# Kernel optimization log

Measured on AMD Instinct MI355X. Metric: run time of the kernel, lower is better.

The kernel has to match this reference:

```python
import jax, jax.numpy as jnp
import numpy as np

NUM_HEADS = 16


def setup_inputs() -> dict:
    key = jax.random.key(0)
    ks = jax.random.split(key, 6)
    B, N, M, C = 2, 2048, 2048, 1024
    return {
        "reference_data": jax.random.normal(ks[0], (B, N, C), dtype=jnp.float32),
        "target_data": jax.random.normal(ks[1], (B, M, C), dtype=jnp.float32),
        "Wq": jax.random.normal(ks[2], (C, C), dtype=jnp.float32) * (C ** -0.5),
        "Wkv": jax.random.normal(ks[3], (C, 2 * C), dtype=jnp.float32) * (C ** -0.5),
        "Wproj": jax.random.normal(ks[4], (C, C), dtype=jnp.float32) * (C ** -0.5),
        "bproj": jnp.zeros((C,), dtype=jnp.float32),
    }


def reference(reference_data, target_data, Wq, Wkv, Wproj, bproj):
    B, N, C = reference_data.shape
    M = target_data.shape[1]
    H = NUM_HEADS
    hd = C // H
    scale = hd ** -0.5
    # k, v from reference: [B, N, 2, H, hd] -> two [B, H, N, hd]
    kv = (reference_data @ Wkv).reshape(B, N, 2, H, hd)
    k = jnp.transpose(kv[:, :, 0], (0, 2, 1, 3))  # [B,H,N,hd]
    v = jnp.transpose(kv[:, :, 1], (0, 2, 1, 3))  # [B,H,N,hd]
    # q from target: [B, H, M, hd]
    q = jnp.transpose((target_data @ Wq).reshape(B, M, H, hd), (0, 2, 1, 3))
    attn = jnp.einsum("bhid,bhjd->bhij", q, k) * scale  # [B,H,M,N]
    attn = jax.nn.softmax(attn, axis=-1)
    x = jnp.einsum("bhij,bhjd->bhid", attn, v)  # [B,H,M,hd]
    x = jnp.transpose(x, (0, 2, 1, 3)).reshape(B, M, C)
    return x @ Wproj + bproj
```

## Files before the change

kernel.cpp:

```cpp
#include <hip/hip_runtime.h>
#include <hip/hip_bf16.h>
#include <stdint.h>

#define SEQ   2048
#define CH    1024
#define NH    16
#define HD    64

typedef short bf8 __attribute__((ext_vector_type(8)));
typedef short bf4 __attribute__((ext_vector_type(4)));
typedef float f4  __attribute__((ext_vector_type(4)));
typedef unsigned short u16;

#define GAS(p) ((const __attribute__((address_space(1))) void*)(p))
#define LAS(p) ((__attribute__((address_space(3))) void*)(p))

__device__ __forceinline__ u16 f2bf(float f) {
  uint32_t u = __float_as_uint(f);
  u += 0x7fffu + ((u >> 16) & 1u);
  return (u16)(u >> 16);
}

__device__ __forceinline__ uint32_t pk2bf(float a, float b) {
  float2 f; f.x = a; f.y = b;
  __hip_bfloat162 h = __float22bfloat162_rn(f);
  union { __hip_bfloat162 h; uint32_t u; } cv; cv.h = h;
  return cv.u;
}

__device__ __forceinline__ f4 MFMA32(bf8 a, bf8 b, f4 c) {
  return __builtin_amdgcn_mfma_f32_16x16x32_bf16(a, b, c, 0, 0, 0);
}

__device__ __forceinline__ f4 MFMA16(bf4 a, bf4 b, f4 c) {
#if __has_builtin(__builtin_amdgcn_mfma_f32_16x16x16_bf16)
  return __builtin_amdgcn_mfma_f32_16x16x16_bf16(a, b, c, 0, 0, 0);
#elif __has_builtin(__builtin_amdgcn_mfma_f32_16x16x16bf16_1k)
  return __builtin_amdgcn_mfma_f32_16x16x16bf16_1k(a, b, c, 0, 0, 0);
#else
  f4 d = c;
  asm volatile("v_mfma_f32_16x16x16_bf16 %0, %1, %2, %0"
               : "+v"(d) : "v"(a), "v"(b));
  return d;
#endif
}

__global__ void prep(const float* __restrict__ ref, u16* __restrict__ refb,
                     const float* __restrict__ tgt, u16* __restrict__ tgtb,
                     const float* __restrict__ Wq, u16* __restrict__ Wqt,
                     const float* __restrict__ Wkv, u16* __restrict__ Wkvt,
                     const float* __restrict__ Wp, u16* __restrict__ Wpt) {
  __shared__ float tile[32][33];
  int blk = blockIdx.x;
  int t = threadIdx.x;
  if (blk < 8192) {
    const float* in; u16* out;
    if (blk < 4096) { in = ref; out = refb; } else { in = tgt; out = tgtb; blk -= 4096; }
    int i = (blk * 256 + t) * 4;
    float4 f = *reinterpret_cast<const float4*>(in + i);
    ushort4 o;
    o.x = f2bf(f.x); o.y = f2bf(f.y); o.z = f2bf(f.z); o.w = f2bf(f.w);
    *reinterpret_cast<ushort4*>(out + i) = o;
    return;
  }
  blk -= 8192;
  int x = blk & 127, by = blk >> 7;
  const float* in; u16* out; int N;
  if (x < 32)       { in = Wq;  out = Wqt;  N = CH;     }
  else if (x < 96)  { in = Wkv; out = Wkvt; N = 2 * CH; x -= 32; }
  else              { in = Wp;  out = Wpt;  N = CH;     x -= 96; }
  const int K = CH;
  int bn = x * 32, bk = by * 32;
  int tx = t & 31, ty = t >> 5;
  #pragma unroll
  for (int i = ty; i < 32; i += 8)
    tile[i][tx] = in[(size_t)(bk + i) * N + bn + tx];
  __syncthreads();
  #pragma unroll
  for (int i = ty; i < 32; i += 8)
    out[(size_t)(bn + i) * K + bk + tx] = f2bf(tile[tx][i]);
}

__global__ __launch_bounds__(256, 3)
void gemm_qkv(const u16* __restrict__ tgtb, const u16* __restrict__ refb,
              const u16* __restrict__ Wqt, const u16* __restrict__ Wkvt,
              u16* __restrict__ qb, u16* __restrict__ karr, u16* __restrict__ varr)
{
  __shared__ __align__(16) u16 As[2][4096];
  __shared__ __align__(16) u16 Bs[2][4096];
  const int tid = threadIdx.x;
  const int lane = tid & 63, wave = tid >> 6;
  const int l16 = lane & 15, q = lane >> 4;
  const bool isQ = blockIdx.x >= 16;
  const u16* A  = isQ ? tgtb : refb;
  const u16* Bt = isQ ? Wqt : Wkvt;
  const int n0 = (isQ ? (blockIdx.x - 16) : blockIdx.x) * 128;
  const int m0 = blockIdx.y * 128;
  const int wm = (wave >> 1) * 64, wn = (wave & 1) * 64;
  const int Kdim = CH;
  const int c = tid, c2 = tid + 256;
  const int ar = c >> 2, ac = (c & 3) << 3, ar2 = c2 >> 2, ac2 = (c2 & 3) << 3;

  f4 acc[4][4] = {};

  #define STAGE_G(buf, k0)                                                      \
    { __builtin_amdgcn_global_load_lds(                                         \
          GAS(&A[(size_t)(m0 + ar) * Kdim + (k0) + ac]),                        \
          LAS(&As[buf][c << 3]), 16, 0, 0);                                     \
      __builtin_amdgcn_global_load_lds(                                         \
          GAS(&A[(size_t)(m0 + ar2) * Kdim + (k0) + ac2]),                      \
          LAS(&As[buf][c2 << 3]), 16, 0, 0);                                    \
      __builtin_amdgcn_global_load_lds(                                         \
          GAS(&Bt[(size_t)(n0 + ar) * Kdim + (k0) + ac]),                       \
          LAS(&Bs[buf][c << 3]), 16, 0, 0);                                     \
      __builtin_amdgcn_global_load_lds(                                         \
          GAS(&Bt[(size_t)(n0 + ar2) * Kdim + (k0) + ac2]),                     \
          LAS(&Bs[buf][c2 << 3]), 16, 0, 0); }

  STAGE_G(0, 0);
  for (int kk = 0; kk < 32; ++kk) {
    __syncthreads();
    if (kk < 31) STAGE_G((kk + 1) & 1, (kk + 1) * 32);
    const u16* as = As[kk & 1];
    const u16* bs = Bs[kk & 1];
    bf8 a[4], b[4];
    #pragma unroll
    for (int i = 0; i < 4; ++i)
      a[i] = *reinterpret_cast<const bf8*>(&as[(wm + i * 16 + l16) * 32 + q * 8]);
    #pragma unroll
    for (int j = 0; j < 4; ++j)
      b[j] = *reinterpret_cast<const bf8*>(&bs[(wn + j * 16 + l16) * 32 + q * 8]);
    #pragma unroll
    for (int i = 0; i < 4; ++i)
      #pragma unroll
      for (int j = 0; j < 4; ++j)
        acc[i][j] = MFMA32(a[i], b[j], acc[i][j]);
  }
  #undef STAGE_G

  #pragma unroll
  for (int i = 0; i < 4; ++i) {
    const int mbase = m0 + wm + i * 16 + q * 4;
    const int b = mbase >> 11, ns0 = mbase & (SEQ - 1);
    #pragma unroll
    for (int j = 0; j < 4; ++j) {
      const int n = n0 + wn + j * 16 + l16;
      if (isQ) {
        int h = n >> 6, d = n & 63;
        #pragma unroll
        for (int r = 0; r < 4; ++r)
          qb[(size_t)((b * NH + h) * SEQ + ns0 + r) * HD + d] =
              f2bf(acc[i][j][r] * 0.1803368801f);
      } else if (n < CH) {
        int h = n >> 6, d = n & 63;
        size_t base = (size_t)(b * NH + h) * SEQ * HD;
        int off = (((ns0 >> 4) * 2 + (d >> 5)) * 4 + ((d >> 3) & 3)) * 128
                  + (d & 7);
        #pragma unroll
        for (int r = 0; r < 4; ++r)
          karr[base + off + ((ns0 + r) & 15) * 8] = f2bf(acc[i][j][r]);
      } else {
        int c2v = n - CH, h = c2v >> 6, d = c2v & 63;
        size_t base = (size_t)(b * NH + h) * SEQ * HD;
        int off = (((ns0 >> 4) * 2 + (d >> 5)) * 4 + ((ns0 >> 2) & 3)) * 128
                  + (d & 15) * 8 + ((d >> 4) & 1) * 4;
        ushort4 st;
        st.x = f2bf(acc[i][j][0]); st.y = f2bf(acc[i][j][1]);
        st.z = f2bf(acc[i][j][2]); st.w = f2bf(acc[i][j][3]);
        *reinterpret_cast<ushort4*>(&varr[base + off]) = st;
      }
    }
  }
}

__global__ __launch_bounds__(256, 2)
void gemm_proj(const u16* __restrict__ A, const u16* __restrict__ Bt,
               float* __restrict__ fo, const float* __restrict__ bias)
{
  __shared__ __align__(16) u16 As[2][2048];
  __shared__ __align__(16) u16 Bs[2][4096];
  const int tid = threadIdx.x;
  const int lane = tid & 63, wave = tid >> 6;
  const int l16 = lane & 15, q = lane >> 4;
  const int m0 = blockIdx.y * 64, n0 = blockIdx.x * 128;
  const int wm = (wave >> 1) * 32, wn = (wave & 1) * 64;
  const int Kdim = CH;
  const int c = tid, c2 = tid + 256;
  const int ar = c >> 2, ac = (c & 3) << 3, ar2 = c2 >> 2, ac2 = (c2 & 3) << 3;

  f4 acc[2][4] = {};

  #define STAGE_P(buf, k0)                                                      \
    { __builtin_amdgcn_global_load_lds(                                         \
          GAS(&A[(size_t)(m0 + (ar >> 1)) * Kdim + (k0) + ((c & 7) << 2) * 2]), \
          LAS(&As[buf][(c & 255) << 3]), 16, 0, 0);                             \
      __builtin_amdgcn_global_load_lds(                                         \
          GAS(&Bt[(size_t)(n0 + ar) * Kdim + (k0) + ac]),                       \
          LAS(&Bs[buf][c << 3]), 16, 0, 0);                                     \
      __builtin_amdgcn_global_load_lds(                                         \
          GAS(&Bt[(size_t)(n0 + ar2) * Kdim + (k0) + ac2]),                     \
          LAS(&Bs[buf][c2 << 3]), 16, 0, 0); }

  #undef STAGE_P
  const int aar = c >> 2;
  const int aac = (c & 3) << 3;
  #define STAGE_P(buf, k0)                                                      \
    { __builtin_amdgcn_global_load_lds(                                         \
          GAS(&A[(size_t)(m0 + aar) * Kdim + (k0) + aac]),                      \
          LAS(&As[buf][c << 3]), 16, 0, 0);                                     \
      __builtin_amdgcn_global_load_lds(                                         \
          GAS(&Bt[(size_t)(n0 + ar) * Kdim + (k0) + ac]),                       \
          LAS(&Bs[buf][c << 3]), 16, 0, 0);                                     \
      __builtin_amdgcn_global_load_lds(                                         \
          GAS(&Bt[(size_t)(n0 + ar2) * Kdim + (k0) + ac2]),                     \
          LAS(&Bs[buf][c2 << 3]), 16, 0, 0); }

  STAGE_P(0, 0);
  for (int kk = 0; kk < 32; ++kk) {
    __syncthreads();
    if (kk < 31) STAGE_P((kk + 1) & 1, (kk + 1) * 32);
    const u16* as = As[kk & 1];
    const u16* bs = Bs[kk & 1];
    bf8 a[2], b[4];
    #pragma unroll
    for (int i = 0; i < 2; ++i)
      a[i] = *reinterpret_cast<const bf8*>(&as[(wm + i * 16 + l16) * 32 + q * 8]);
    #pragma unroll
    for (int j = 0; j < 4; ++j)
      b[j] = *reinterpret_cast<const bf8*>(&bs[(wn + j * 16 + l16) * 32 + q * 8]);
    #pragma unroll
    for (int i = 0; i < 2; ++i)
      #pragma unroll
      for (int j = 0; j < 4; ++j)
        acc[i][j] = MFMA32(a[i], b[j], acc[i][j]);
  }
  #undef STAGE_P

  #pragma unroll
  for (int i = 0; i < 2; ++i) {
    const int mbase = m0 + wm + i * 16 + q * 4;
    #pragma unroll
    for (int j = 0; j < 4; ++j) {
      const int n = n0 + wn + j * 16 + l16;
      #pragma unroll
      for (int r = 0; r < 4; ++r)
        fo[(size_t)(mbase + r) * CH + n] = acc[i][j][r] + bias[n];
    }
  }
}

__global__ __launch_bounds__(512, 4)
void attn(const u16* __restrict__ Q, const u16* __restrict__ Karr,
          const u16* __restrict__ Varr, u16* __restrict__ X)
{
  __shared__ __align__(16) u16 Ks[2][8192];
  __shared__ __align__(16) u16 Vs[2][8192];
  const int tid = threadIdx.x;
  const int lane = tid & 63;
  const int l16 = lane & 15, q = lane >> 4;
  const int bh = blockIdx.y;
  const int m0 = blockIdx.x * 128;
  const int wm = (tid >> 6) * 16;

  const u16* Qb = Q    + (size_t)bh * SEQ * HD;
  const u16* Kb = Karr + (size_t)bh * SEQ * HD;
  const u16* Vb = Varr + (size_t)bh * SEQ * HD;

  bf8 qf[2];
  #pragma unroll
  for (int ks = 0; ks < 2; ++ks)
    qf[ks] = *reinterpret_cast<const bf8*>(
        &Qb[(size_t)(m0 + wm + l16) * HD + ks * 32 + q * 8]);

  const short one_bf = 0x3F80;
  const bf4 ones = {one_bf, one_bf, one_bf, one_bf};

  f4 o[4] = {};
  f4 ds = {};

  #define STAGE_A(buf, t)                                                       \
    { const u16* kg = Kb + (size_t)(t) * 8192;                                  \
      const u16* vg = Vb + (size_t)(t) * 8192;                                  \
      _Pragma("unroll")                                                         \
      for (int s = 0; s < 2; ++s) {                                             \
        int cc = tid + s * 512;                                                 \
        __builtin_amdgcn_global_load_lds(GAS(kg + cc * 8),                      \
                                         LAS(&Ks[buf][cc * 8]), 16, 0, 0);      \
        __builtin_amdgcn_global_load_lds(GAS(vg + cc * 8),                      \
                                         LAS(&Vs[buf][cc * 8]), 16, 0, 0);      \
      } }

  STAGE_A(0, 0);
  for (int t = 0; t < SEQ / 128; ++t) {
    __syncthreads();
    if (t < SEQ / 128 - 1) STAGE_A((t + 1) & 1, t + 1);
    const u16* ks = Ks[t & 1];
    const u16* vs = Vs[t & 1];

    bf4 pa[8];
    #pragma unroll
    for (int j = 0; j < 8; ++j) {
      bf8 kf0 = *reinterpret_cast<const bf8*>(&ks[((j * 2 + 0) * 4 + q) * 128 + l16 * 8]);
      bf8 kf1 = *reinterpret_cast<const bf8*>(&ks[((j * 2 + 1) * 4 + q) * 128 + l16 * 8]);
      f4 z = {};
      z = MFMA32(kf0, qf[0], z);
      z = MFMA32(kf1, qf[1], z);
      union { bf4 v; uint32_t u[2]; } w;
      w.u[0] = pk2bf(exp2f(z[0]), exp2f(z[1]));
      w.u[1] = pk2bf(exp2f(z[2]), exp2f(z[3]));
      pa[j] = w.v;
    }

    #pragma unroll
    for (int j = 0; j < 8; ++j) {
      ds = MFMA16(pa[j], ones, ds);
      #pragma unroll
      for (int dh = 0; dh < 2; ++dh) {
        bf8 vv = *reinterpret_cast<const bf8*>(&vs[((j * 2 + dh) * 4 + q) * 128 + l16 * 8]);
        bf4 v0 = __builtin_shufflevector(vv, vv, 0, 1, 2, 3);
        bf4 v1 = __builtin_shufflevector(vv, vv, 4, 5, 6, 7);
        o[dh * 2 + 0] = MFMA16(pa[j], v0, o[dh * 2 + 0]);
        o[dh * 2 + 1] = MFMA16(pa[j], v1, o[dh * 2 + 1]);
      }
    }
  }
  #undef STAGE_A

  const int b = bh >> 4, h = bh & (NH - 1);
  #pragma unroll
  for (int r = 0; r < 4; ++r) {
    float ir = 1.0f / ds[r];
    int m = m0 + wm + q * 4 + r;
    #pragma unroll
    for (int dt = 0; dt < 4; ++dt) {
      int d = dt * 16 + l16;
      X[(size_t)(b * SEQ + m) * CH + h * HD + d] = f2bf(o[dt][r] * ir);
    }
  }
}

extern "C" void kernel_launch(void* const* d_in, const int* in_sizes, int n_in,
                              void* d_out, int out_size, void* d_ws, size_t ws_size,
                              hipStream_t stream) {
  const float* ref   = (const float*)d_in[0];
  const float* tgt   = (const float*)d_in[1];
  const float* Wq    = (const float*)d_in[2];
  const float* Wkv   = (const float*)d_in[3];
  const float* Wproj = (const float*)d_in[4];
  const float* bproj = (const float*)d_in[5];
  float* out = (float*)d_out;

  char* ws = (char*)d_ws;
  u16* refb = (u16*)(ws);
  u16* tgtb = (u16*)(ws + (8  << 20));
  u16* Wqt  = (u16*)(ws + (16 << 20));
  u16* Wkvt = (u16*)(ws + (18 << 20));
  u16* Wpt  = (u16*)(ws + (22 << 20));
  u16* qb   = (u16*)(ws + (24 << 20));
  u16* karr = (u16*)(ws + (32 << 20));
  u16* varr = (u16*)(ws + (40 << 20));
  u16* xb   = (u16*)(ws + (48 << 20));

  prep<<<12288, 256, 0, stream>>>(ref, refb, tgt, tgtb, Wq, Wqt, Wkv, Wkvt, Wproj, Wpt);

  gemm_qkv<<<dim3(24, 32), 256, 0, stream>>>(tgtb, refb, Wqt, Wkvt, qb, karr, varr);

  attn<<<dim3(16, 32), 512, 0, stream>>>(qb, karr, varr, xb);

  gemm_proj<<<dim3(8, 64), 256, 0, stream>>>(xb, Wpt, out, bproj);
}
```

Measured before the change: 215.3 us.

## Split attention over two KV halves and merge with a combine kernel

The attention kernel gains a grid z-dimension of 2, so each block processes half of the key/value sequence with half-size LDS tiles, and launch bounds now allow more blocks per CU. Each half writes a normalized partial output and its row sum to workspace. A new combine kernel then merges the two halves weighted by their sums into the head-interleaved layout. The aim is more parallelism and occupancy in the attention stage, paid for with an extra launch, extra global traffic for the partials, and one more bf16 rounding step.

```diff
diff --git a/kernel.cpp b/kernel.cpp
--- a/kernel.cpp
+++ b/kernel.cpp
@@ -19,6 +19,10 @@
   uint32_t u = __float_as_uint(f);
   u += 0x7fffu + ((u >> 16) & 1u);
   return (u16)(u >> 16);
+}
+
+__device__ __forceinline__ float bf2f(u16 v) {
+  return __uint_as_float(((uint32_t)v) << 16);
 }
 
 __device__ __forceinline__ uint32_t pk2bf(float a, float b) {
@@ -190,18 +194,6 @@
 
   f4 acc[2][4] = {};
 
-  #define STAGE_P(buf, k0)                                                      \
-    { __builtin_amdgcn_global_load_lds(                                         \
-          GAS(&A[(size_t)(m0 + (ar >> 1)) * Kdim + (k0) + ((c & 7) << 2) * 2]), \
-          LAS(&As[buf][(c & 255) << 3]), 16, 0, 0);                             \
-      __builtin_amdgcn_global_load_lds(                                         \
-          GAS(&Bt[(size_t)(n0 + ar) * Kdim + (k0) + ac]),                       \
-          LAS(&Bs[buf][c << 3]), 16, 0, 0);                                     \
-      __builtin_amdgcn_global_load_lds(                                         \
-          GAS(&Bt[(size_t)(n0 + ar2) * Kdim + (k0) + ac2]),                     \
-          LAS(&Bs[buf][c2 << 3]), 16, 0, 0); }
-
-  #undef STAGE_P
   const int aar = c >> 2;
   const int aac = (c & 3) << 3;
   #define STAGE_P(buf, k0)                                                      \
@@ -249,28 +241,30 @@
   }
 }
 
-__global__ __launch_bounds__(512, 4)
+__global__ __launch_bounds__(512, 8)
 void attn(const u16* __restrict__ Q, const u16* __restrict__ Karr,
-          const u16* __restrict__ Varr, u16* __restrict__ X)
+          const u16* __restrict__ Varr, u16* __restrict__ XP,
+          float* __restrict__ DS)
 {
-  __shared__ __align__(16) u16 Ks[2][8192];
-  __shared__ __align__(16) u16 Vs[2][8192];
+  __shared__ __align__(16) u16 Ks[2][4096];
+  __shared__ __align__(16) u16 Vs[2][4096];
   const int tid = threadIdx.x;
   const int lane = tid & 63;
   const int l16 = lane & 15, q = lane >> 4;
   const int bh = blockIdx.y;
+  const int z = blockIdx.z;
   const int m0 = blockIdx.x * 128;
   const int wm = (tid >> 6) * 16;
 
   const u16* Qb = Q    + (size_t)bh * SEQ * HD;
-  const u16* Kb = Karr + (size_t)bh * SEQ * HD;
-  const u16* Vb = Varr + (size_t)bh * SEQ * HD;
+  const u16* Kb = Karr + (size_t)bh * SEQ * HD + (size_t)z * 1024 * HD;
+  const u16* Vb = Varr + (size_t)bh * SEQ * HD + (size_t)z * 1024 * HD;
 
   bf8 qf[2];
   #pragma unroll
-  for (int ks = 0; ks < 2; ++ks)
-    qf[ks] = *reinterpret_cast<const bf8*>(
-        &Qb[(size_t)(m0 + wm + l16) * HD + ks * 32 + q * 8]);
+  for (int s = 0; s < 2; ++s)
+    qf[s] = *reinterpret_cast<const bf8*>(
+        &Qb[(size_t)(m0 + wm + l16) * HD + s * 32 + q * 8]);
 
   const short one_bf = 0x3F80;
   const bf4 ones = {one_bf, one_bf, one_bf, one_bf};
@@ -278,41 +272,35 @@
   f4 o[4] = {};
   f4 ds = {};
 
-  #define STAGE_A(buf, t)                                                       \
-    { const u16* kg = Kb + (size_t)(t) * 8192;                                  \
-      const u16* vg = Vb + (size_t)(t) * 8192;                                  \
-      _Pragma("unroll")                                                         \
-      for (int s = 0; s < 2; ++s) {                                             \
-        int cc = tid + s * 512;                                                 \
-        __builtin_amdgcn_global_load_lds(GAS(kg + cc * 8),                      \
-                                         LAS(&Ks[buf][cc * 8]), 16, 0, 0);      \
-        __builtin_amdgcn_global_load_lds(GAS(vg + cc * 8),                      \
-                                         LAS(&Vs[buf][cc * 8]), 16, 0, 0);      \
-      } }
+  #define STAGE_A(buf, t)                                                     \
+    { __builtin_amdgcn_global_load_lds(GAS(Kb + (size_t)(t) * 4096 + tid * 8),\
+                                       LAS(&Ks[buf][tid * 8]), 16, 0, 0);     \
+      __builtin_amdgcn_global_load_lds(GAS(Vb + (size_t)(t) * 4096 + tid * 8),\
+                                       LAS(&Vs[buf][tid * 8]), 16, 0, 0); }
 
   STAGE_A(0, 0);
-  for (int t = 0; t < SEQ / 128; ++t) {
+  for (int t = 0; t < 16; ++t) {
     __syncthreads();
-    if (t < SEQ / 128 - 1) STAGE_A((t + 1) & 1, t + 1);
+    if (t < 15) STAGE_A((t + 1) & 1, t + 1);
     const u16* ks = Ks[t & 1];
     const u16* vs = Vs[t & 1];
 
-    bf4 pa[8];
-    #pragma unroll
-    for (int j = 0; j < 8; ++j) {
+    bf4 pa[4];
+    #pragma unroll
+    for (int j = 0; j < 4; ++j) {
       bf8 kf0 = *reinterpret_cast<const bf8*>(&ks[((j * 2 + 0) * 4 + q) * 128 + l16 * 8]);
       bf8 kf1 = *reinterpret_cast<const bf8*>(&ks[((j * 2 + 1) * 4 + q) * 128 + l16 * 8]);
-      f4 z = {};
-      z = MFMA32(kf0, qf[0], z);
-      z = MFMA32(kf1, qf[1], z);
+      f4 zf = {};
+      zf = MFMA32(kf0, qf[0], zf);
+      zf = MFMA32(kf1, qf[1], zf);
       union { bf4 v; uint32_t u[2]; } w;
-      w.u[0] = pk2bf(exp2f(z[0]), exp2f(z[1]));
-      w.u[1] = pk2bf(exp2f(z[2]), exp2f(z[3]));
+      w.u[0] = pk2bf(exp2f(zf[0]), exp2f(zf[1]));
+      w.u[1] = pk2bf(exp2f(zf[2]), exp2f(zf[3]));
       pa[j] = w.v;
     }
 
     #pragma unroll
-    for (int j = 0; j < 8; ++j) {
+    for (int j = 0; j < 4; ++j) {
       ds = MFMA16(pa[j], ones, ds);
       #pragma unroll
       for (int dh = 0; dh < 2; ++dh) {
@@ -326,17 +314,42 @@
   }
   #undef STAGE_A
 
-  const int b = bh >> 4, h = bh & (NH - 1);
   #pragma unroll
   for (int r = 0; r < 4; ++r) {
     float ir = 1.0f / ds[r];
     int m = m0 + wm + q * 4 + r;
+    size_t row = (size_t)(z * NH * 2 + bh) * SEQ + m;
+    if (l16 == 0) DS[row] = ds[r];
     #pragma unroll
     for (int dt = 0; dt < 4; ++dt) {
       int d = dt * 16 + l16;
-      X[(size_t)(b * SEQ + m) * CH + h * HD + d] = f2bf(o[dt][r] * ir);
-    }
-  }
+      XP[row * HD + d] = f2bf(o[dt][r] * ir);
+    }
+  }
+}
+
+__global__ __launch_bounds__(256)
+void combine(const u16* __restrict__ XP, const float* __restrict__ DS,
+             u16* __restrict__ xb)
+{
+  const int t = threadIdx.x;
+  const int row = blockIdx.x * 16 + (t >> 4);
+  const int d0 = (t & 15) * 4;
+  const float s0 = DS[row], s1 = DS[65536 + row];
+  const float inv = 1.0f / (s0 + s1);
+  const float w0 = s0 * inv, w1 = s1 * inv;
+  ushort4 a = *reinterpret_cast<const ushort4*>(&XP[(size_t)row * HD + d0]);
+  ushort4 b4 = *reinterpret_cast<const ushort4*>(
+      &XP[(size_t)(65536 + row) * HD + d0]);
+  ushort4 o;
+  o.x = f2bf(w0 * bf2f(a.x) + w1 * bf2f(b4.x));
+  o.y = f2bf(w0 * bf2f(a.y) + w1 * bf2f(b4.y));
+  o.z = f2bf(w0 * bf2f(a.z) + w1 * bf2f(b4.z));
+  o.w = f2bf(w0 * bf2f(a.w) + w1 * bf2f(b4.w));
+  const int bh = row >> 11, m = row & (SEQ - 1);
+  const int b = bh >> 4, h = bh & (NH - 1);
+  *reinterpret_cast<ushort4*>(
+      &xb[(size_t)(b * SEQ + m) * CH + h * HD + d0]) = o;
 }
 
 extern "C" void kernel_launch(void* const* d_in, const int* in_sizes, int n_in,
@@ -360,12 +373,16 @@
   u16* karr = (u16*)(ws + (32 << 20));
   u16* varr = (u16*)(ws + (40 << 20));
   u16* xb   = (u16*)(ws + (48 << 20));
+  u16*   XP = (u16*)(ws);
+  float* DS = (float*)(ws + (16 << 20));
 
   prep<<<12288, 256, 0, stream>>>(ref, refb, tgt, tgtb, Wq, Wqt, Wkv, Wkvt, Wproj, Wpt);
 
   gemm_qkv<<<dim3(24, 32), 256, 0, stream>>>(tgtb, refb, Wqt, Wkvt, qb, karr, varr);
 
-  attn<<<dim3(16, 32), 512, 0, stream>>>(qb, karr, varr, xb);
+  attn<<<dim3(16, 32, 2), 512, 0, stream>>>(qb, karr, varr, XP, DS);
+
+  combine<<<4096, 256, 0, stream>>>(XP, DS, xb);
 
   gemm_proj<<<dim3(8, 64), 256, 0, stream>>>(xb, Wpt, out, bproj);
 }
```

Measured after the change: 223.1 us. 1.04x slower.
